# Kernel tuning notes

Measured on AMD Instinct MI355X. Metric: run time of the kernel, lower is better.

## Reference

```python
import jax, jax.numpy as jnp
import numpy as np

N_FFT = 1024
HOP = 256
WIN_LEN = N_FFT  # win_length == n_fft
PAD = (WIN_LEN - HOP) // 2  # 'same' padding


def hann_window(n):
    # torch.hann_window default (periodic=True): 0.5*(1-cos(2*pi*k/n))
    k = jnp.arange(n, dtype=jnp.float32)
    return 0.5 * (1.0 - jnp.cos(2.0 * jnp.pi * k / n))


def setup_inputs() -> dict:
    key = jax.random.key(0)
    k1, k2 = jax.random.split(key)
    B, L, D = 8, 2048, 512
    x = jax.random.normal(k1, (B, L, D), dtype=jnp.float32)
    W = jax.random.normal(k2, (D, N_FFT + 2), dtype=jnp.float32) * (1.0 / np.sqrt(D))
    b = jnp.zeros((N_FFT + 2,), dtype=jnp.float32)
    return {"x": x, "W": W, "b": b}


def reference(x, W, b):
    # Linear projection: (B, L, n_fft+2)
    h = jnp.einsum("bld,do->blo", x, W) + b
    nbins = N_FFT // 2 + 1  # 513
    mag = jnp.minimum(jnp.exp(h[..., :nbins]), 100.0)  # exp + clip max=100
    p = h[..., nbins:]
    # Complex STFT coefficients S: (B, L, nbins)
    S = mag * (jnp.cos(p) + 1j * jnp.sin(p))
    # Per-frame inverse rFFT (norm='backward' = default): (B, L, n_fft)
    frames = jnp.fft.irfft(S, n=N_FFT, axis=-1)
    win = hann_window(WIN_LEN)
    frames = frames * win  # windowed frames
    B, T = frames.shape[0], frames.shape[1]
    out_size = (T - 1) * HOP + WIN_LEN
    # Overlap-add via scatter-add
    idx = jnp.arange(T)[:, None] * HOP + jnp.arange(WIN_LEN)[None, :]  # (T, n_fft)
    y = jnp.zeros((B, out_size), dtype=frames.dtype).at[:, idx].add(frames)
    env = jnp.zeros((out_size,), dtype=frames.dtype).at[idx].add(
        jnp.broadcast_to(win * win, (T, WIN_LEN))
    )
    y = y[:, PAD:-PAD] / env[PAD:-PAD]
    return y
```

## Files before the change

### kernel.cpp

```cpp
#include <hip/hip_runtime.h>
#include <math.h>


using half8 = __attribute__((ext_vector_type(8))) _Float16;
using f32x4 = __attribute__((ext_vector_type(4))) float;

#define TWO_PI_OVER_1024 0.006135923151542565f

#define OFF_A2 0
#define OFF_B2 35651584UL
#define OFF_A1 37879808UL
#define OFF_B1 54657024UL
#define OFF_FR 37879808UL

__device__ __forceinline__ float hannf(int s) {
    return 0.5f * (1.0f - __cosf(TWO_PI_OVER_1024 * (float)s));
}

__device__ __forceinline__ void stage16(const void* g, void* lds) {
    __builtin_amdgcn_global_load_lds(
        (const __attribute__((address_space(1))) void*)g,
        (__attribute__((address_space(3))) void*)lds,
        16, 0, 0);
}

__global__ __launch_bounds__(256)
void prep_k(const float* __restrict__ x, const float* __restrict__ W,
            _Float16* __restrict__ A1, _Float16* __restrict__ B1,
            _Float16* __restrict__ B2)
{
    const int bid = blockIdx.x;
    if (bid < 4096) {
        const size_t tid = (size_t)bid * 256 + threadIdx.x;
        const int l   = (int)(tid & 63);
        const size_t f = tid >> 6;
        const int mts = (int)(f & 7);
        const size_t g = f >> 3;
        const int kt  = (int)(g & 15);
        const int mtb = (int)(g >> 4);
        const int m   = mtb * 128 + mts * 16 + (l & 15);
        const int k0  = kt * 32 + (l >> 4) * 8;
        const float* xp = x + (size_t)m * 512 + k0;
        const float4 v0 = *(const float4*)xp;
        const float4 v1 = *(const float4*)(xp + 4);
        const float vv[8] = {v0.x, v0.y, v0.z, v0.w, v1.x, v1.y, v1.z, v1.w};
        half8 o;
#pragma unroll
        for (int j = 0; j < 8; ++j) o[j] = (_Float16)vv[j];
        *(half8*)(A1 + tid * 8) = o;
    } else if (bid < 4384) {
        const int tid = (bid - 4096) * 256 + threadIdx.x;
        const int l  = tid & 63;
        const int f  = tid >> 6;
        const int t8 = f & 7;
        const int g  = f >> 3;
        const int kt = g & 15;
        const int bx = g >> 4;
        const int side = t8 >> 2;
        const int nt   = t8 & 3;
        const int c    = bx * 64 + nt * 16 + (l & 15);
        const int k0   = kt * 32 + (l >> 4) * 8;
        const int wcol = side ? (513 + c) : c;
        half8 o;
#pragma unroll
        for (int j = 0; j < 8; ++j) {
            float v = (c < 513) ? W[(size_t)(k0 + j) * 1026 + wcol] : 0.0f;
            o[j] = (_Float16)v;
        }
        *(half8*)(B1 + (size_t)tid * 8) = o;
    } else {
        const int tid = (bid - 4384) * 256 + threadIdx.x;
        const int l  = tid & 63;
        const int f  = tid >> 6;
        const int nt = f % 6;
        const int g  = f / 6;
        const int kt = g % 34;
        const int nblk = g / 34;
        const int n  = nblk * 96 + nt * 16 + (l & 15);
        const int kk0 = kt * 32 + (l >> 4) * 8;
        const float win = hannf(n) * (1.0f / 1024.0f);
        half8 o;
#pragma unroll
        for (int j = 0; j < 8; ++j) {
            const int kk = kk0 + j;
            float v = 0.0f;
            if (kk < 544) {
                const int k = kk;
                if (k < 513) {
                    const float coef = (k == 0 || k == 512) ? 1.0f : 2.0f;
                    v = coef * __cosf(TWO_PI_OVER_1024 * (float)((k * n) & 1023)) * win;
                }
            } else {
                const int k = kk - 544;
                if (k < 513) {
                    const float coef = (k == 0 || k == 512) ? 1.0f : 2.0f;
                    v = -coef * __sinf(TWO_PI_OVER_1024 * (float)((k * n) & 1023)) * win;
                }
            }
            o[j] = (_Float16)v;
        }
        *(half8*)(B2 + (size_t)tid * 8) = o;
    }
}


__global__ __launch_bounds__(256, 4)
void gemm1_k(const _Float16* __restrict__ A, const _Float16* __restrict__ B,
             const float* __restrict__ bias, _Float16* __restrict__ A2)
{
    __shared__ _Float16 Ash[2][8 * 512];
    __shared__ _Float16 Bsh[2][8 * 512];
    const int t = threadIdx.x, w = t >> 6, l = t & 63;

    const int lin = blockIdx.x;
    const int xcd = lin & 7, slot = lin >> 3;
    const int mblk = xcd * 16 + slot / 9;
    const int bx   = slot % 9;

    const int wm = (w & 1) * 4;
    const int q  = w >> 1;
    const int jt[4] = {2 * q, 2 * q + 1, 4 + 2 * q, 5 + 2 * q};

    f32x4 acc[4][4];
#pragma unroll
    for (int i = 0; i < 4; ++i)
#pragma unroll
        for (int j = 0; j < 4; ++j) acc[i][j] = (f32x4)0.0f;

    const int lane8 = l * 8;
    const _Float16* Ab = A + ((size_t)mblk * 16 * 8) * 512 + lane8;
    const _Float16* Bb = B + ((size_t)bx * 16 * 8) * 512 + lane8;

    for (int step = 0; step < 8; ++step) {
        const int kt0 = 2 * step;
        __syncthreads();
#pragma unroll
        for (int i = 0; i < 4; ++i) {
            const int s = 4 * w + i;
            const int u = s >> 3, r = s & 7;
            stage16(Ab + ((size_t)(kt0 + u) * 8 + r) * 512, &Ash[u][r * 512]);
            stage16(Bb + ((size_t)(kt0 + u) * 8 + r) * 512, &Bsh[u][r * 512]);
        }
        __syncthreads();

#pragma unroll
        for (int u = 0; u < 2; ++u) {
            half8 a[4], b[4];
#pragma unroll
            for (int i = 0; i < 4; ++i)
                a[i] = *(const half8*)&Ash[u][(wm + i) * 512 + lane8];
#pragma unroll
            for (int j = 0; j < 4; ++j)
                b[j] = *(const half8*)&Bsh[u][jt[j] * 512 + lane8];
#pragma unroll
            for (int i = 0; i < 4; ++i)
#pragma unroll
                for (int j = 0; j < 4; ++j)
                    acc[i][j] = __builtin_amdgcn_mfma_f32_16x16x32_f16(a[i], b[j], acc[i][j], 0, 0, 0);
        }
    }

    _Float16* SrT = &Ash[0][0];
    _Float16* SiT = &Bsh[0][0];

    __syncthreads();
    const int r4 = (l >> 4) * 4, c16 = l & 15;
#pragma unroll
    for (int i = 0; i < 4; ++i) {
        const int row0 = (wm + i) * 16 + r4;
#pragma unroll
        for (int p = 0; p < 2; ++p) {
            const int cl = (2 * q + p) * 16 + c16;
            const int c  = bx * 64 + cl;
            const bool valid = (c < 513);
            const float bm = valid ? bias[c] : 0.0f;
            const float bp = valid ? bias[513 + c] : 0.0f;
#pragma unroll
            for (int r = 0; r < 4; ++r) {
                float Sr = 0.0f, Si = 0.0f;
                if (valid) {
                    const float mag = fminf(__expf(acc[i][p][r] + bm), 100.0f);
                    const float ph  = acc[i][2 + p][r] + bp;
                    Sr = mag * __cosf(ph);
                    Si = mag * __sinf(ph);
                }
                const int row = row0 + r;
                const int idx = row * 64 + (cl ^ ((row & 7) * 8));
                SrT[idx] = (_Float16)Sr;
                SiT[idx] = (_Float16)Si;
            }
        }
    }
    __syncthreads();

#pragma unroll
    for (int f = 0; f < 4; ++f) {
        const int tau  = w * 4 + f;
        const int kt2l = tau >> 3, mts = tau & 7;
        if (bx * 2 + kt2l < 17) {
            const int row = mts * 16 + (l & 15);
            const int kl  = kt2l * 32 + (l >> 4) * 8;
            const int idx = row * 64 + (kl ^ ((row & 7) * 8));
            const half8 vr = *(const half8*)&SrT[idx];
            const half8 vi = *(const half8*)&SiT[idx];
            const int ktr = bx * 2 + kt2l;
            const int kti = 17 + ktr;
            *(half8*)(A2 + ((((size_t)mblk * 34 + ktr) * 8 + mts) * 64 + l) * 8) = vr;
            *(half8*)(A2 + ((((size_t)mblk * 34 + kti) * 8 + mts) * 64 + l) * 8) = vi;
        }
    }
}


__device__ __forceinline__ void mma43(const _Float16* __restrict__ As,
                                      const _Float16* __restrict__ Bs,
                                      int wm, int wn, int lane16, f32x4 (&acc)[4][3])
{
    half8 a[4], b[3];
#pragma unroll
    for (int i = 0; i < 4; ++i) a[i] = *(const half8*)&As[(wm + i) * 512 + lane16];
#pragma unroll
    for (int j = 0; j < 3; ++j) b[j] = *(const half8*)&Bs[(wn + j) * 512 + lane16];
#pragma unroll
    for (int i = 0; i < 4; ++i)
#pragma unroll
        for (int j = 0; j < 3; ++j)
            acc[i][j] = __builtin_amdgcn_mfma_f32_16x16x32_f16(a[i], b[j], acc[i][j], 0, 0, 0);
}

__global__ __launch_bounds__(256, 3)
void gemm2_k(const _Float16* __restrict__ A, const _Float16* __restrict__ Bas,
             _Float16* __restrict__ C)
{
    __shared__ _Float16 As[2][8 * 512];
    __shared__ _Float16 Bs[2][6 * 512];
    const int t = threadIdx.x, w = t >> 6, l = t & 63;

    const int lin = blockIdx.x;
    const int xcd = lin & 7, slot = lin >> 3;
    const int mblk = xcd * 16 + slot / 6;
    const int nblk = slot % 6;

    const int wm = (w & 1) * 4, wn = (w >> 1) * 3;

    f32x4 accC[4][3], accD[4][3];
#pragma unroll
    for (int i = 0; i < 4; ++i)
#pragma unroll
        for (int j = 0; j < 3; ++j) { accC[i][j] = (f32x4)0.0f; accD[i][j] = (f32x4)0.0f; }

    const int lane16 = l * 8;

    for (int step = 0; step < 17; ++step) {
        const int kt0 = 2 * step;
        __syncthreads();
#pragma unroll
        for (int i = 0; i < 4; ++i) {
            const int ta = 4 * w + i;
            const int u = ta >> 3, mts = ta & 7;
            const _Float16* Ag = A + ((((size_t)mblk * 34 + (kt0 + u)) * 8 + mts) * 512) + lane16;
            stage16(Ag, &As[u][mts * 512]);
        }
#pragma unroll
        for (int i = 0; i < 3; ++i) {
            const int tb = 3 * w + i;
            const int u = tb / 6, nt = tb % 6;
            const _Float16* Bg = Bas + ((((size_t)nblk * 34 + (kt0 + u)) * 6 + nt) * 512) + lane16;
            stage16(Bg, &Bs[u][nt * 512]);
        }
        __syncthreads();

#pragma unroll
        for (int u = 0; u < 2; ++u) {
            const int kt = kt0 + u;
            if (kt < 17) mma43(As[u], Bs[u], wm, wn, lane16, accC);
            else         mma43(As[u], Bs[u], wm, wn, lane16, accD);
        }
    }

    const int r4 = (l >> 4) * 4, c0 = l & 15;
#pragma unroll
    for (int i = 0; i < 4; ++i) {
        const int m = mblk * 128 + (wm + i) * 16 + r4;
#pragma unroll
        for (int j = 0; j < 3; ++j) {
            const int n = nblk * 96 + (wn + j) * 16 + c0;
#pragma unroll
            for (int r = 0; r < 4; ++r) {
                const float cv = accC[i][j][r];
                const float dv = accD[i][j][r];
                _Float16* row = C + (size_t)(m + r) * 1024;
                if (n < 513)           row[n]        = (_Float16)(cv + dv);
                if (n >= 1 && n < 512) row[1024 - n] = (_Float16)(cv - dv);
            }
        }
    }
}


__global__ __launch_bounds__(256)
void ola_kernel(const _Float16* __restrict__ frames, float* __restrict__ out)
{
    const int idx = blockIdx.x * 256 + threadIdx.x;
    const int b = idx >> 19;
    const int j = idx & 524287;
    const int n = j + 384;

    int t_hi = n >> 8;
    if (t_hi > 2047) t_hi = 2047;
    const int t_lo = (n >= 1023) ? ((n - 1023 + 255) >> 8) : 0;

    float acc = 0.0f, env = 0.0f;
    for (int tt = t_lo; tt <= t_hi; ++tt) {
        const int s = n - (tt << 8);
        const float wv = hannf(s);
        acc += (float)frames[(((size_t)(b * 2048 + tt)) << 10) + s];
        env += wv * wv;
    }
    out[idx] = acc / env;
}


extern "C" void kernel_launch(void* const* d_in, const int* in_sizes, int n_in,
                              void* d_out, int out_size, void* d_ws, size_t ws_size,
                              hipStream_t stream)
{
    const float* x = (const float*)d_in[0];
    const float* W = (const float*)d_in[1];
    const float* b = (const float*)d_in[2];
    float* out = (float*)d_out;
    char* ws = (char*)d_ws;

    _Float16* A2 = (_Float16*)(ws + OFF_A2);
    _Float16* B2 = (_Float16*)(ws + OFF_B2);
    _Float16* A1 = (_Float16*)(ws + OFF_A1);
    _Float16* B1 = (_Float16*)(ws + OFF_B1);
    _Float16* frames = (_Float16*)(ws + OFF_FR);

    prep_k<<<4690, 256, 0, stream>>>(x, W, A1, B1, B2);

    gemm1_k<<<1152, 256, 0, stream>>>(A1, B1, b, A2);
    gemm2_k<<<768, 256, 0, stream>>>(A2, B2, frames);

    ola_kernel<<<out_size / 256, 256, 0, stream>>>(frames, out);
}
```

Before: 162.0 us.

## Stage gemm2 output through LDS, split frames into halves, vectorize overlap-add

The gemm2 epilogue now writes its accumulators into LDS and then emits coalesced half8 stores into two buffers: the first-half frame samples (FL, row stride 576) and the mirrored second half (FH, stride 512). Before, it did scattered scalar stores straight into the full 1024-sample frames. The overlap-add kernel now has each thread produce 8 outputs, reading four half8 vectors from the FL/FH layout. In the interior it replaces the per-sample Hann envelope division with a constant 2/3 factor, and it keeps the general loop only near the edges. This cuts uncoalesced global traffic in both kernels, at the cost of extra LDS syncs and more complicated index and edge handling.

```diff
diff --git a/kernel.cpp b/kernel.cpp
--- a/kernel.cpp
+++ b/kernel.cpp
@@ -11,7 +11,8 @@
 #define OFF_B2 35651584UL
 #define OFF_A1 37879808UL
 #define OFF_B1 54657024UL
-#define OFF_FR 37879808UL
+#define OFF_FL 37879808UL
+#define OFF_FH 56754176UL
 
 __device__ __forceinline__ float hannf(int s) {
     return 0.5f * (1.0f - __cosf(TWO_PI_OVER_1024 * (float)s));
@@ -230,10 +231,11 @@
 
 __global__ __launch_bounds__(256, 3)
 void gemm2_k(const _Float16* __restrict__ A, const _Float16* __restrict__ Bas,
-             _Float16* __restrict__ C)
-{
-    __shared__ _Float16 As[2][8 * 512];
-    __shared__ _Float16 Bs[2][6 * 512];
+             _Float16* __restrict__ FL, _Float16* __restrict__ FH)
+{
+    __shared__ _Float16 SH[14336];
+    _Float16* As0 = SH;
+    _Float16* Bs0 = SH + 8192;
     const int t = threadIdx.x, w = t >> 6, l = t & 63;
 
     const int lin = blockIdx.x;
@@ -259,65 +261,130 @@
             const int ta = 4 * w + i;
             const int u = ta >> 3, mts = ta & 7;
             const _Float16* Ag = A + ((((size_t)mblk * 34 + (kt0 + u)) * 8 + mts) * 512) + lane16;
-            stage16(Ag, &As[u][mts * 512]);
+            stage16(Ag, &As0[u * 4096 + mts * 512]);
         }
 #pragma unroll
         for (int i = 0; i < 3; ++i) {
             const int tb = 3 * w + i;
             const int u = tb / 6, nt = tb % 6;
             const _Float16* Bg = Bas + ((((size_t)nblk * 34 + (kt0 + u)) * 6 + nt) * 512) + lane16;
-            stage16(Bg, &Bs[u][nt * 512]);
+            stage16(Bg, &Bs0[u * 3072 + nt * 512]);
         }
         __syncthreads();
 
 #pragma unroll
         for (int u = 0; u < 2; ++u) {
             const int kt = kt0 + u;
-            if (kt < 17) mma43(As[u], Bs[u], wm, wn, lane16, accC);
-            else         mma43(As[u], Bs[u], wm, wn, lane16, accD);
+            if (kt < 17) mma43(As0 + u * 4096, Bs0 + u * 3072, wm, wn, lane16, accC);
+            else         mma43(As0 + u * 4096, Bs0 + u * 3072, wm, wn, lane16, accD);
         }
     }
 
     const int r4 = (l >> 4) * 4, c0 = l & 15;
+    __syncthreads();
 #pragma unroll
     for (int i = 0; i < 4; ++i) {
-        const int m = mblk * 128 + (wm + i) * 16 + r4;
+        const int row = (wm + i) * 16 + r4;
+#pragma unroll
+        for (int j = 0; j < 3; ++j) {
+            const int lcol = (wn + j) * 16 + c0;
+#pragma unroll
+            for (int r = 0; r < 4; ++r)
+                SH[(row + r) * 104 + lcol] = (_Float16)(accC[i][j][r] + accD[i][j][r]);
+        }
+    }
+    __syncthreads();
+    for (int qq = t; qq < 1536; qq += 256) {
+        const int row = qq / 12, cc = qq % 12;
+        const half8 v = *(const half8*)&SH[row * 104 + cc * 8];
+        *(half8*)(FL + (size_t)(mblk * 128 + row) * 576 + nblk * 96 + cc * 8) = v;
+    }
+    __syncthreads();
+
+    const int Cbase = (nblk == 5) ? 0 : (416 - 96 * nblk);
+    const int lo = (nblk == 5) ? 0 : 1;
+    const int hi = (nblk == 0) ? 95 : ((nblk == 5) ? 32 : 96);
+#pragma unroll
+    for (int i = 0; i < 4; ++i) {
+        const int row = (wm + i) * 16 + r4;
 #pragma unroll
         for (int j = 0; j < 3; ++j) {
             const int n = nblk * 96 + (wn + j) * 16 + c0;
 #pragma unroll
             for (int r = 0; r < 4; ++r) {
-                const float cv = accC[i][j][r];
-                const float dv = accD[i][j][r];
-                _Float16* row = C + (size_t)(m + r) * 1024;
-                if (n < 513)           row[n]        = (_Float16)(cv + dv);
-                if (n >= 1 && n < 512) row[1024 - n] = (_Float16)(cv - dv);
+                if (n >= 1 && n <= 511)
+                    SH[(row + r) * 104 + (512 - n - Cbase)] =
+                        (_Float16)(accC[i][j][r] - accD[i][j][r]);
+                else if (n == 512)
+                    SH[(row + r) * 104 + 0] =
+                        (_Float16)(accC[i][j][r] + accD[i][j][r]);
             }
         }
     }
+    __syncthreads();
+    for (int qq = t; qq < 1664; qq += 256) {
+        const int row = qq / 13, cc = qq % 13;
+        if (8 * cc > hi) continue;
+        _Float16* dst = FH + (size_t)(mblk * 128 + row) * 512 + Cbase + 8 * cc;
+        if (8 * cc >= lo && 8 * cc + 7 <= hi) {
+            *(half8*)dst = *(const half8*)&SH[row * 104 + cc * 8];
+        } else {
+#pragma unroll
+            for (int e = 0; e < 8; ++e) {
+                const int lc = 8 * cc + e;
+                if (lc >= lo && lc <= hi) dst[e] = SH[row * 104 + lc];
+            }
+        }
+    }
 }
 
 
 __global__ __launch_bounds__(256)
-void ola_kernel(const _Float16* __restrict__ frames, float* __restrict__ out)
-{
-    const int idx = blockIdx.x * 256 + threadIdx.x;
-    const int b = idx >> 19;
-    const int j = idx & 524287;
-    const int n = j + 384;
-
-    int t_hi = n >> 8;
-    if (t_hi > 2047) t_hi = 2047;
-    const int t_lo = (n >= 1023) ? ((n - 1023 + 255) >> 8) : 0;
-
-    float acc = 0.0f, env = 0.0f;
-    for (int tt = t_lo; tt <= t_hi; ++tt) {
-        const int s = n - (tt << 8);
-        const float wv = hannf(s);
-        acc += (float)frames[(((size_t)(b * 2048 + tt)) << 10) + s];
-        env += wv * wv;
-    }
-    out[idx] = acc / env;
+void ola_kernel(const _Float16* __restrict__ FL, const _Float16* __restrict__ FH,
+                float* __restrict__ out)
+{
+    const int gid = blockIdx.x * 256 + threadIdx.x;
+    const size_t base = (size_t)gid * 8;
+    const int b  = (int)(base >> 19);
+    const int j0 = (int)(base & 524287);
+    const int n0 = j0 + 384;
+
+    if (j0 >= 640 && j0 < 523904) {
+        const int nb = n0 & 255;
+        const int T  = n0 >> 8;
+        const size_t mT = (size_t)b * 2048 + T;
+        const half8 v0 = *(const half8*)(FL + (mT    ) * 576 + nb);
+        const half8 v1 = *(const half8*)(FL + (mT - 1) * 576 + nb + 256);
+        const half8 v2 = *(const half8*)(FH + (mT - 2) * 512 + nb);
+        const half8 v3 = *(const half8*)(FH + (mT - 3) * 512 + nb + 256);
+        f32x4 o0, o1;
+#pragma unroll
+        for (int e = 0; e < 4; ++e)
+            o0[e] = ((float)v0[e] + (float)v1[e] + (float)v2[e] + (float)v3[e]) * (2.0f / 3.0f);
+#pragma unroll
+        for (int e = 0; e < 4; ++e)
+            o1[e] = ((float)v0[4 + e] + (float)v1[4 + e] + (float)v2[4 + e] + (float)v3[4 + e]) * (2.0f / 3.0f);
+        *(f32x4*)(out + base) = o0;
+        *(f32x4*)(out + base + 4) = o1;
+    } else {
+        for (int e = 0; e < 8; ++e) {
+            const int n = n0 + e;
+            int t_hi = n >> 8;
+            if (t_hi > 2047) t_hi = 2047;
+            const int t_lo = (n >= 1023) ? ((n - 768) >> 8) : 0;
+            float acc = 0.0f, env = 0.0f;
+            for (int tt = t_lo; tt <= t_hi; ++tt) {
+                const int s = n - (tt << 8);
+                const float wv = hannf(s);
+                const size_t m = (size_t)b * 2048 + tt;
+                const float fv = (s < 512) ? (float)FL[m * 576 + s]
+                                           : (float)FH[m * 512 + (s - 512)];
+                acc += fv;
+                env += wv * wv;
+            }
+            out[base + e] = acc / env;
+        }
+    }
 }
 
 
@@ -335,12 +402,13 @@
     _Float16* B2 = (_Float16*)(ws + OFF_B2);
     _Float16* A1 = (_Float16*)(ws + OFF_A1);
     _Float16* B1 = (_Float16*)(ws + OFF_B1);
-    _Float16* frames = (_Float16*)(ws + OFF_FR);
+    _Float16* FL = (_Float16*)(ws + OFF_FL);
+    _Float16* FH = (_Float16*)(ws + OFF_FH);
 
     prep_k<<<4690, 256, 0, stream>>>(x, W, A1, B1, B2);
 
     gemm1_k<<<1152, 256, 0, stream>>>(A1, B1, b, A2);
-    gemm2_k<<<768, 256, 0, stream>>>(A2, B2, frames);
-
-    ola_kernel<<<out_size / 256, 256, 0, stream>>>(frames, out);
-}
+    gemm2_k<<<768, 256, 0, stream>>>(A2, B2, FL, FH);
+
+    ola_kernel<<<out_size / 2048, 256, 0, stream>>>(FL, FH, out);
+}
```

New measurement: 164.9 us, median of 2. About the same (+1.8%).
